# Optimization experiments

Hardware: AMD Instinct MI355X
Metric: run time of the kernel (lower is better)

## Reference

```python
import jax, jax.numpy as jnp
import numpy as np

N = 50000
E = 800000
BN_EPS = 1e-5


def setup_inputs() -> dict:
    key = jax.random.key(0)
    ks = jax.random.split(key, 8)
    x = jax.random.normal(ks[0], (N, 64), dtype=jnp.float32)
    edge_index = jax.random.randint(ks[1], (2, E), 0, N, dtype=jnp.int64)
    edge_attr = jax.random.uniform(ks[2], (E,), dtype=jnp.float32)
    # GraphConv layer 1: lin_rel (with bias) + lin_root (no bias), 64 -> 128
    W1_rel = jax.random.normal(ks[3], (64, 128), dtype=jnp.float32) / np.sqrt(64)
    b1 = jnp.zeros((128,), dtype=jnp.float32)
    W1_root = jax.random.normal(ks[4], (64, 128), dtype=jnp.float32) / np.sqrt(64)
    # BatchNorm1d(128) affine params
    gamma = jnp.ones((128,), dtype=jnp.float32)
    beta = jnp.zeros((128,), dtype=jnp.float32)
    # GraphConv layer 2: 128 -> 32
    W2_rel = jax.random.normal(ks[5], (128, 32), dtype=jnp.float32) / np.sqrt(128)
    b2 = jnp.zeros((32,), dtype=jnp.float32)
    W2_root = jax.random.normal(ks[6], (128, 32), dtype=jnp.float32) / np.sqrt(128)
    return {"x": x, "edge_attr": edge_attr, "W1_rel": W1_rel, "b1": b1,
            "W1_root": W1_root, "gamma": gamma, "beta": beta,
            "W2_rel": W2_rel, "b2": b2, "W2_root": W2_root,
            "edge_index": edge_index}


def graph_conv(x, edge_index, edge_weight, W_rel, b_rel, W_root):
    # PyG GraphConv (aggr='add'): out = lin_rel(scatter_add(w_e * x[src] -> dst)) + lin_root(x)
    src, dst = edge_index[0], edge_index[1]
    msg = x[src] * edge_weight[:, None]              # [E, F] gather + scale
    agg = jax.ops.segment_sum(msg, dst, num_segments=x.shape[0])  # [N, F]
    return agg @ W_rel + b_rel + x @ W_root


def batch_norm_train(h, gamma, beta):
    mean = jnp.mean(h, axis=0)
    var = jnp.var(h, axis=0)  # biased, as torch uses for normalization
    return (h - mean) * jax.lax.rsqrt(var + BN_EPS) * gamma + beta


def reference(x, edge_attr, W1_rel, b1, W1_root, gamma, beta, W2_rel, b2, W2_root, edge_index):
    h = graph_conv(x, edge_index, edge_attr, W1_rel, b1, W1_root)
    h = batch_norm_train(h, gamma, beta)
    h = jnp.tanh(h)
    out = graph_conv(h, edge_index, edge_attr, W2_rel, b2, W2_root)
    return out
```

## Files before the change

### kernel.cpp

```cpp
#include <hip/hip_runtime.h>
#include <hip/hip_bf16.h>


#define NB 256
#define CAPB 4096
#define LCAP 16
#define CHUNK 2048
#define CAP 32
#define MAXROWS 196
#define OVF_CAP 131072

typedef __bf16 bf16x8 __attribute__((ext_vector_type(8)));
typedef float f32x4 __attribute__((ext_vector_type(4)));

__device__ __forceinline__ void atomAdd(float* p, float v) { unsafeAtomicAdd(p, v); }

__device__ __forceinline__ unsigned packrec(unsigned src, float w) {
    __bf16 bw = (__bf16)w;
    unsigned short us = *(unsigned short*)&bw;
    return (src << 16) | (unsigned)us;
}

__global__ __launch_bounds__(256) void cvtw_k(
    const float* __restrict__ W1rel, const float* __restrict__ W1root,
    const float* __restrict__ W2rel, const float* __restrict__ W2root,
    const float* __restrict__ x,
    __bf16* __restrict__ W1t, __bf16* __restrict__ W2t, __bf16* __restrict__ xb,
    int* __restrict__ gcnt, int* __restrict__ ovfcnt,
    float* __restrict__ bnsum, float* __restrict__ bnsq, int N) {
    if (blockIdx.x == 0) {
        int t = threadIdx.x;
        if (t < NB) gcnt[t] = 0;
        if (t == 0) *ovfcnt = 0;
        if (t < 128) { bnsum[t] = 0.f; bnsq[t] = 0.f; }
    }
    int idx = blockIdx.x * 256 + threadIdx.x;
    if (idx < 128 * 128) {
        int n = idx >> 7, k = idx & 127;
        float v = (k < 64) ? W1rel[k * 128 + n] : W1root[(k - 64) * 128 + n];
        W1t[n * 128 + k] = (__bf16)v;
    } else if (idx < 128 * 128 + 64 * 128) {
        int j = idx - 128 * 128;
        int n = j >> 7, k = j & 127;
        float v = (n < 32) ? W2rel[k * 32 + n] : W2root[k * 32 + (n - 32)];
        W2t[n * 128 + k] = (__bf16)v;
    } else {
        int j = idx - (128 * 128 + 64 * 128);
        if (j < N * 8) {
            const float4* xs = (const float4*)(x + (size_t)j * 8);
            float4 a = xs[0], b = xs[1];
            bf16x8 v;
            v[0] = (__bf16)a.x; v[1] = (__bf16)a.y; v[2] = (__bf16)a.z; v[3] = (__bf16)a.w;
            v[4] = (__bf16)b.x; v[5] = (__bf16)b.y; v[6] = (__bf16)b.z; v[7] = (__bf16)b.w;
            *(bf16x8*)(xb + (size_t)j * 8) = v;
        }
    }
}

__global__ __launch_bounds__(256) void part_k(
    const float* __restrict__ ea, const void* __restrict__ ei,
    int* __restrict__ gcnt, uint2* __restrict__ part,
    int* __restrict__ ovfcnt, int4* __restrict__ ovf, int E, int N) {
    __shared__ int s_flag;
    __shared__ int hist[NB];
    __shared__ int gb[NB];
    __shared__ uint2 stage[NB * LCAP];

    if (threadIdx.x < 64) {
        const long long* p = (const long long*)ei;
        long long v = p[threadIdx.x & 15];
        int ok = (v >= 0 && v < (long long)N);
        unsigned long long m = __ballot(ok);
        if (threadIdx.x == 0) s_flag = (~m == 0ull) ? 1 : 0;
    }
    for (int i = threadIdx.x; i < NB; i += 256) hist[i] = 0;
    __syncthreads();
    const bool is64 = (s_flag != 0);

    const int base = blockIdx.x * CHUNK + threadIdx.x * 8;
    int n = E - base; n = n < 0 ? 0 : (n > 8 ? 8 : n);

    int srcs[8], dsts[8]; float wv[8];
    if (n > 0) {
        if (is64) {
            const long long* p = (const long long*)ei;
            if (n == 8 && ((E & 1) == 0)) {
#pragma unroll
                for (int k = 0; k < 4; k++) {
                    int4 a = *(const int4*)(p + base + 2 * k);
                    srcs[2 * k] = a.x; srcs[2 * k + 1] = a.z;
                }
#pragma unroll
                for (int k = 0; k < 4; k++) {
                    int4 b = *(const int4*)(p + E + base + 2 * k);
                    dsts[2 * k] = b.x; dsts[2 * k + 1] = b.z;
                }
            } else {
                for (int k = 0; k < n; k++) { srcs[k] = (int)p[base + k]; dsts[k] = (int)p[E + base + k]; }
            }
        } else {
            const int* p = (const int*)ei;
            if (n == 8 && ((E & 3) == 0)) {
                int4 a0 = *(const int4*)(p + base);
                int4 a1 = *(const int4*)(p + base + 4);
                srcs[0] = a0.x; srcs[1] = a0.y; srcs[2] = a0.z; srcs[3] = a0.w;
                srcs[4] = a1.x; srcs[5] = a1.y; srcs[6] = a1.z; srcs[7] = a1.w;
                int4 b0 = *(const int4*)(p + E + base);
                int4 b1 = *(const int4*)(p + E + base + 4);
                dsts[0] = b0.x; dsts[1] = b0.y; dsts[2] = b0.z; dsts[3] = b0.w;
                dsts[4] = b1.x; dsts[5] = b1.y; dsts[6] = b1.z; dsts[7] = b1.w;
            } else {
                for (int k = 0; k < n; k++) { srcs[k] = p[base + k]; dsts[k] = p[E + base + k]; }
            }
        }
        if (n == 8) {
            float4 w0 = *(const float4*)(ea + base);
            float4 w1 = *(const float4*)(ea + base + 4);
            wv[0] = w0.x; wv[1] = w0.y; wv[2] = w0.z; wv[3] = w0.w;
            wv[4] = w1.x; wv[5] = w1.y; wv[6] = w1.z; wv[7] = w1.w;
        } else {
            for (int k = 0; k < n; k++) wv[k] = ea[base + k];
        }

        int bk[8], pos[8], loc[8];
#pragma unroll
        for (int k = 0; k < 8; k++) {
            if (k < n) {
                unsigned b = ((unsigned)dsts[k] << 8) / (unsigned)N;
                int r0 = (int)((b * (unsigned)N + 255u) >> 8);
                bk[k] = (int)b;
                loc[k] = dsts[k] - r0;
                pos[k] = atomicAdd(&hist[b], 1);
            }
        }
#pragma unroll
        for (int k = 0; k < 8; k++) {
            if (k < n) {
                unsigned packed = ((unsigned)loc[k] << 24) | (unsigned)srcs[k];
                if (pos[k] < LCAP) {
                    stage[bk[k] * LCAP + pos[k]] = make_uint2(packed, __float_as_uint(wv[k]));
                } else {
                    int g = atomicAdd(&gcnt[bk[k]], 1);
                    if (g < CAPB) {
                        part[(size_t)bk[k] * CAPB + g] = make_uint2(packed, __float_as_uint(wv[k]));
                    } else {
                        int o = atomicAdd(ovfcnt, 1);
                        if (o < OVF_CAP) ovf[o] = make_int4(srcs[k], dsts[k], (int)__float_as_uint(wv[k]), 0);
                    }
                }
            }
        }
    }
    __syncthreads();
    if (threadIdx.x < NB) {
        int h = hist[threadIdx.x]; if (h > LCAP) h = LCAP;
        hist[threadIdx.x] = h;
        gb[threadIdx.x] = h ? atomicAdd(&gcnt[threadIdx.x], h) : 0;
    }
    __syncthreads();
    const int wvi = threadIdx.x >> 6;
    const int sub = (threadIdx.x >> 4) & 3;
    const int f = threadIdx.x & 15;
    for (int round = 0; round < 16; ++round) {
        int b = wvi * 64 + round * 4 + sub;
        int h = hist[b];
        if (f < h) {
            int g = gb[b] + f;
            uint2 r = stage[b * LCAP + f];
            if (g < CAPB) {
                part[(size_t)b * CAPB + g] = r;
            } else {
                int r0 = (b * N + 255) >> 8;
                int dst = r0 + (int)(r.x >> 24);
                int o = atomicAdd(ovfcnt, 1);
                if (o < OVF_CAP) ovf[o] = make_int4((int)(r.x & 0xFFFFFFu), dst, (int)r.y, 0);
            }
        }
    }
}

__global__ __launch_bounds__(256) void binscat_k(
    const int* __restrict__ gcnt, const uint2* __restrict__ part,
    unsigned* __restrict__ bins, int* __restrict__ cnt,
    int* __restrict__ ovfcnt, int4* __restrict__ ovf, int N) {
    __shared__ unsigned stage[MAXROWS * CAP];
    __shared__ int lcnt[MAXROWS];
    const int b = blockIdx.x;
    const int r0 = (b * N + 255) >> 8;
    int r1 = ((b + 1) * N + 255) >> 8; if (r1 > N) r1 = N;
    const int rows = r1 - r0;
    for (int i = threadIdx.x; i < rows; i += 256) lcnt[i] = 0;
    __syncthreads();

    int m = gcnt[b]; if (m > CAPB) m = CAPB;
    const uint2* pb = part + (size_t)b * CAPB;
    for (int i = threadIdx.x; i < m; i += 256) {
        uint2 r = pb[i];
        int d = r.x >> 24;
        unsigned src = r.x & 0xFFFFFFu;
        float w = __uint_as_float(r.y);
        int pos = atomicAdd(&lcnt[d], 1);
        if (pos < CAP) {
            stage[d * CAP + pos] = packrec(src, w);
        } else {
            int o = atomicAdd(ovfcnt, 1);
            if (o < OVF_CAP) ovf[o] = make_int4((int)src, r0 + d, (int)r.y, 0);
        }
    }
    __syncthreads();
    uint4* dst = (uint4*)(bins + (size_t)r0 * CAP);
    const uint4* srcp = (const uint4*)stage;
    for (int i = threadIdx.x; i < rows * (CAP / 4); i += 256) dst[i] = srcp[i];
    for (int i = threadIdx.x; i < rows; i += 256) cnt[r0 + i] = lcnt[i];
}

__global__ __launch_bounds__(256) void spmm1_k(
    const __bf16* __restrict__ xb, const int* __restrict__ cntg,
    const unsigned* __restrict__ bins, const int* __restrict__ ovfcnt,
    const int4* __restrict__ ovf, __bf16* __restrict__ aggb, int N) {
    const int lane = threadIdx.x & 63;
    const int row = (blockIdx.x * 256 + threadIdx.x) >> 6;
    if (row >= N) return;
    int cf = cntg[row];
    int cnt = cf > CAP ? CAP : cf;
    unsigned eg = 0u;
    if (lane < cnt) eg = bins[(size_t)row * CAP + lane];
    float acc = 0.f;
    for (int j = 0; j < cnt; j += 8) {
        int s[8]; float w[8], v[8];
#pragma unroll
        for (int k = 0; k < 8; k++) {
            int idx = j + k;
            bool ok = idx < cnt;
            unsigned r = (unsigned)__shfl((int)eg, idx);
            s[k] = ok ? (int)(r >> 16) : 0;
            w[k] = ok ? __uint_as_float((r & 0xFFFFu) << 16) : 0.f;
        }
#pragma unroll
        for (int k = 0; k < 8; k++) v[k] = (float)xb[(size_t)s[k] * 64 + lane];
#pragma unroll
        for (int k = 0; k < 8; k++) acc = fmaf(w[k], v[k], acc);
    }
    if (cf > CAP) {
        int nv = *ovfcnt; if (nv > OVF_CAP) nv = OVF_CAP;
        for (int i = 0; i < nv; i++) {
            int4 t = ovf[i];
            if (t.y == row) {
                float w = __uint_as_float((unsigned)t.z);
                acc = fmaf(w, (float)xb[(size_t)t.x * 64 + lane], acc);
            }
        }
    }
    aggb[(size_t)row * 64 + lane] = (__bf16)acc;
}

__global__ __launch_bounds__(256) void gemm1_k(
    const __bf16* __restrict__ aggb, const __bf16* __restrict__ xb,
    const __bf16* __restrict__ W1t, const float* __restrict__ b1,
    __bf16* __restrict__ hb, float* __restrict__ bnsum, float* __restrict__ bnsq,
    int N) {
    __shared__ char Wl[128 * 256];
    __shared__ float redS[4][128];
    __shared__ float redQ[4][128];
    const int t = threadIdx.x;
    for (int i = t; i < 2048; i += 256) {
        int byte = i * 16;
        int row = byte >> 8;
        int sw = byte ^ ((row & 7) << 4);
        *(uint4*)(Wl + sw) = *(const uint4*)((const char*)W1t + byte);
    }

    const int lane = t & 63;
    const int w = t >> 6;
    const int rrow = lane & 15;
    const int q = lane >> 4;
    const int rowbase = blockIdx.x * 128 + w * 32;
    const int ar0 = rowbase + rrow;
    const int ar1 = rowbase + 16 + rrow;
    const int ar0c = (ar0 < N) ? ar0 : (N - 1);
    const int ar1c = (ar1 < N) ? ar1 : (N - 1);

    f32x4 acc0[8], acc1[8];
#pragma unroll
    for (int cb = 0; cb < 8; cb++) {
        acc0[cb][0] = 0.f; acc0[cb][1] = 0.f; acc0[cb][2] = 0.f; acc0[cb][3] = 0.f;
        acc1[cb][0] = 0.f; acc1[cb][1] = 0.f; acc1[cb][2] = 0.f; acc1[cb][3] = 0.f;
    }
    __syncthreads();

#pragma unroll
    for (int ks = 0; ks < 4; ks++) {
        const int koff = (ks & 1) * 32 + q * 8;
        const __bf16* base = (ks < 2) ? aggb : xb;
        bf16x8 a0 = *(const bf16x8*)(base + (size_t)ar0c * 64 + koff);
        bf16x8 a1 = *(const bf16x8*)(base + (size_t)ar1c * 64 + koff);
#pragma unroll
        for (int cb = 0; cb < 8; cb++) {
            int byte = (cb * 16 + rrow) * 256 + ks * 64 + q * 16;
            byte ^= ((rrow & 7) << 4);
            bf16x8 b = *(const bf16x8*)(Wl + byte);
            acc0[cb] = __builtin_amdgcn_mfma_f32_16x16x32_bf16(a0, b, acc0[cb], 0, 0, 0);
            acc1[cb] = __builtin_amdgcn_mfma_f32_16x16x32_bf16(a1, b, acc1[cb], 0, 0, 0);
        }
    }

    float s[8], qs[8];
#pragma unroll
    for (int cb = 0; cb < 8; cb++) {
        const int col = cb * 16 + rrow;
        const float bc = b1[col];
        float ls = 0.f, lq = 0.f;
#pragma unroll
        for (int r = 0; r < 4; r++) {
            int rr0 = rowbase + 4 * q + r;
            if (rr0 < N) {
                float v = acc0[cb][r] + bc;
                hb[(size_t)rr0 * 128 + col] = (__bf16)v;
                ls += v; lq += v * v;
            }
            int rr1 = rowbase + 16 + 4 * q + r;
            if (rr1 < N) {
                float v = acc1[cb][r] + bc;
                hb[(size_t)rr1 * 128 + col] = (__bf16)v;
                ls += v; lq += v * v;
            }
        }
        s[cb] = ls; qs[cb] = lq;
    }
#pragma unroll
    for (int cb = 0; cb < 8; cb++) {
        s[cb] += __shfl_xor(s[cb], 16);  s[cb] += __shfl_xor(s[cb], 32);
        qs[cb] += __shfl_xor(qs[cb], 16); qs[cb] += __shfl_xor(qs[cb], 32);
    }
    if (q == 0) {
#pragma unroll
        for (int cb = 0; cb < 8; cb++) {
            redS[w][cb * 16 + rrow] = s[cb];
            redQ[w][cb * 16 + rrow] = qs[cb];
        }
    }
    __syncthreads();
    if (t < 128) {
        atomAdd(&bnsum[t], redS[0][t] + redS[1][t] + redS[2][t] + redS[3][t]);
    } else {
        int c = t - 128;
        atomAdd(&bnsq[c], redQ[0][c] + redQ[1][c] + redQ[2][c] + redQ[3][c]);
    }
}

__global__ __launch_bounds__(256) void gemm2_k(
    const __bf16* __restrict__ hb, const float* __restrict__ bnsum,
    const float* __restrict__ bnsq, const float* __restrict__ gamma,
    const float* __restrict__ beta, const __bf16* __restrict__ W2t,
    const float* __restrict__ b2, __bf16* __restrict__ y2b,
    float* __restrict__ out, int N) {
    __shared__ char Wl[64 * 256];
    __shared__ float scs[128], shs[128];
    const int t = threadIdx.x;
    for (int i = t; i < 1024; i += 256) {
        int byte = i * 16;
        int row = byte >> 8;
        int sw = byte ^ ((row & 7) << 4);
        *(uint4*)(Wl + sw) = *(const uint4*)((const char*)W2t + byte);
    }
    if (t < 128) {
        float inv = 1.0f / (float)N;
        float mean = bnsum[t] * inv;
        float var = bnsq[t] * inv - mean * mean;
        if (var < 0.f) var = 0.f;
        float sc = gamma[t] * rsqrtf(var + 1e-5f);
        scs[t] = sc;
        shs[t] = beta[t] - mean * sc;
    }

    const int lane = t & 63;
    const int w = t >> 6;
    const int rrow = lane & 15;
    const int q = lane >> 4;
    const int rowbase = blockIdx.x * 128 + w * 32;
    const int ar0 = rowbase + rrow;
    const int ar1 = rowbase + 16 + rrow;
    const int ar0c = (ar0 < N) ? ar0 : (N - 1);
    const int ar1c = (ar1 < N) ? ar1 : (N - 1);

    f32x4 acc0[4], acc1[4];
#pragma unroll
    for (int cb = 0; cb < 4; cb++) {
        acc0[cb][0] = 0.f; acc0[cb][1] = 0.f; acc0[cb][2] = 0.f; acc0[cb][3] = 0.f;
        acc1[cb][0] = 0.f; acc1[cb][1] = 0.f; acc1[cb][2] = 0.f; acc1[cb][3] = 0.f;
    }
    __syncthreads();

#pragma unroll
    for (int ks = 0; ks < 4; ks++) {
        const int k0 = ks * 32 + q * 8;
        bf16x8 hv0 = *(const bf16x8*)(hb + (size_t)ar0c * 128 + k0);
        bf16x8 hv1 = *(const bf16x8*)(hb + (size_t)ar1c * 128 + k0);
        bf16x8 a0, a1;
#pragma unroll
        for (int i = 0; i < 8; i++) {
            float sc = scs[k0 + i], sh = shs[k0 + i];
            a0[i] = (__bf16)tanhf(fmaf((float)hv0[i], sc, sh));
            a1[i] = (__bf16)tanhf(fmaf((float)hv1[i], sc, sh));
        }
#pragma unroll
        for (int cb = 0; cb < 4; cb++) {
            int byte = (cb * 16 + rrow) * 256 + ks * 64 + q * 16;
            byte ^= ((rrow & 7) << 4);
            bf16x8 b = *(const bf16x8*)(Wl + byte);
            acc0[cb] = __builtin_amdgcn_mfma_f32_16x16x32_bf16(a0, b, acc0[cb], 0, 0, 0);
            acc1[cb] = __builtin_amdgcn_mfma_f32_16x16x32_bf16(a1, b, acc1[cb], 0, 0, 0);
        }
    }

#pragma unroll
    for (int cb = 0; cb < 4; cb++) {
        const int col = cb * 16 + rrow;
        const bool isRel = (col < 32);
        const int cc = isRel ? col : (col - 32);
        const float bc = isRel ? 0.f : b2[cc];
#pragma unroll
        for (int r = 0; r < 4; r++) {
            int rr0 = rowbase + 4 * q + r;
            if (rr0 < N) {
                if (isRel) y2b[(size_t)rr0 * 32 + cc] = (__bf16)acc0[cb][r];
                else       out[(size_t)rr0 * 32 + cc] = acc0[cb][r] + bc;
            }
            int rr1 = rowbase + 16 + 4 * q + r;
            if (rr1 < N) {
                if (isRel) y2b[(size_t)rr1 * 32 + cc] = (__bf16)acc1[cb][r];
                else       out[(size_t)rr1 * 32 + cc] = acc1[cb][r] + bc;
            }
        }
    }
}

__global__ __launch_bounds__(256) void spmm2_k(
    const __bf16* __restrict__ y2b, const int* __restrict__ cntg,
    const unsigned* __restrict__ bins, const int* __restrict__ ovfcnt,
    const int4* __restrict__ ovf, float* __restrict__ out, int N) {
    const int lane = threadIdx.x & 63;
    const int f = lane & 31;
    const int sub = lane >> 5;
    const int row = (blockIdx.x * 256 + threadIdx.x) >> 6;
    if (row >= N) return;
    int cf = cntg[row];
    int cnt = cf > CAP ? CAP : cf;
    unsigned eg = 0u;
    if (lane < cnt) eg = bins[(size_t)row * CAP + lane];
    float acc = 0.f;
    for (int j = 0; j < cnt; j += 4) {
        int s[2]; float w[2], v[2];
#pragma unroll
        for (int k = 0; k < 2; k++) {
            int idx = j + 2 * k + sub;
            bool ok = idx < cnt;
            unsigned r = (unsigned)__shfl((int)eg, idx);
            s[k] = ok ? (int)(r >> 16) : 0;
            w[k] = ok ? __uint_as_float((r & 0xFFFFu) << 16) : 0.f;
        }
#pragma unroll
        for (int k = 0; k < 2; k++) v[k] = (float)y2b[(size_t)s[k] * 32 + f];
#pragma unroll
        for (int k = 0; k < 2; k++) acc = fmaf(w[k], v[k], acc);
    }
    if (cf > CAP && sub == 0) {
        int nv = *ovfcnt; if (nv > OVF_CAP) nv = OVF_CAP;
        for (int i = 0; i < nv; i++) {
            int4 t = ovf[i];
            if (t.y == row) {
                float w = __uint_as_float((unsigned)t.z);
                acc = fmaf(w, (float)y2b[(size_t)t.x * 32 + f], acc);
            }
        }
    }
    acc += __shfl_xor(acc, 32);
    if (sub == 0) {
        float* p = &out[(size_t)row * 32 + f];
        *p = *p + acc;
    }
}

extern "C" void kernel_launch(void* const* d_in, const int* in_sizes, int n_in,
                              void* d_out, int out_size, void* d_ws, size_t ws_size,
                              hipStream_t stream) {
    const float* x      = (const float*)d_in[0];
    const float* ea     = (const float*)d_in[1];
    const float* W1rel  = (const float*)d_in[2];
    const float* b1     = (const float*)d_in[3];
    const float* W1root = (const float*)d_in[4];
    const float* gamma  = (const float*)d_in[5];
    const float* beta   = (const float*)d_in[6];
    const float* W2rel  = (const float*)d_in[7];
    const float* b2     = (const float*)d_in[8];
    const float* W2root = (const float*)d_in[9];
    const void*  ei     = d_in[10];

    const int N = in_sizes[0] / 64;
    const int E = in_sizes[1];
    const int nbg = (N + 127) / 128;

    char* ws = (char*)d_ws;
    size_t off = 0;
    int*      gcnt    = (int*)     (ws + off); off += NB * 4;
    int*      ovfcnt  = (int*)     (ws + off); off += 256;
    float*    bnsum   = (float*)   (ws + off); off += 512;
    float*    bnsq    = (float*)   (ws + off); off += 512;
    int*      cnt     = (int*)     (ws + off); off += ((size_t)N * 4 + 255) & ~255ull;
    __bf16*   xb      = (__bf16*)  (ws + off); off += (size_t)N * 64 * 2;
    __bf16*   aggb    = (__bf16*)  (ws + off); off += (size_t)N * 64 * 2;
    __bf16*   hb      = (__bf16*)  (ws + off); off += (size_t)N * 128 * 2;
    __bf16*   y2b     = (__bf16*)  (ws + off); off += (size_t)N * 32 * 2;
    uint2*    part    = (uint2*)   (ws + off); off += (size_t)NB * CAPB * 8;
    unsigned* bins    = (unsigned*)(ws + off); off += (size_t)N * CAP * 4;
    int4*     ovf     = (int4*)    (ws + off); off += (size_t)OVF_CAP * 16;
    __bf16*   W1t     = (__bf16*)  (ws + off); off += 128 * 128 * 2;
    __bf16*   W2t     = (__bf16*)  (ws + off); off += 64 * 128 * 2;

    const int cvtThreads = 128 * 128 + 64 * 128 + N * 8;
    cvtw_k<<<(cvtThreads + 255) / 256, 256, 0, stream>>>(
        W1rel, W1root, W2rel, W2root, x, W1t, W2t, xb, gcnt, ovfcnt, bnsum, bnsq, N);
    part_k<<<(E + CHUNK - 1) / CHUNK, 256, 0, stream>>>(ea, ei, gcnt, part, ovfcnt, ovf, E, N);
    binscat_k<<<NB, 256, 0, stream>>>(gcnt, part, bins, cnt, ovfcnt, ovf, N);
    const int rowBlocks = (N * 64 + 255) / 256;
    spmm1_k<<<rowBlocks, 256, 0, stream>>>(xb, cnt, bins, ovfcnt, ovf, aggb, N);
    gemm1_k<<<nbg, 256, 0, stream>>>(aggb, xb, W1t, b1, hb, bnsum, bnsq, N);
    gemm2_k<<<nbg, 256, 0, stream>>>(hb, bnsum, bnsq, gamma, beta, W2t, b2, y2b,
                                     (float*)d_out, N);
    spmm2_k<<<rowBlocks, 256, 0, stream>>>(y2b, cnt, bins, ovfcnt, ovf, (float*)d_out, N);
}
```

Measured before the change: 117.6 us.

## Vectorize SpMM gathers to packed bf16 pairs and merge x conversion into partition kernel

Both SpMM kernels now load two bf16 features per lane as one 32-bit word and split the wavefront into sub-groups that handle different edges in parallel, then combine the partial sums with cross-lane shuffles. This cuts the number of gather instructions and widens each memory access. The x-to-bf16 conversion moves out of the weight-init kernel into extra leading blocks of the partition kernel, so that conversion can overlap with edge partitioning. The cost is extra shuffle reductions, and the conversion blocks enlarge a launch that also uses a lot of shared memory.

```diff
diff --git a/kernel.cpp b/kernel.cpp
--- a/kernel.cpp
+++ b/kernel.cpp
@@ -21,13 +21,12 @@
     return (src << 16) | (unsigned)us;
 }
 
-__global__ __launch_bounds__(256) void cvtw_k(
+__global__ __launch_bounds__(256) void init_k(
     const float* __restrict__ W1rel, const float* __restrict__ W1root,
     const float* __restrict__ W2rel, const float* __restrict__ W2root,
-    const float* __restrict__ x,
-    __bf16* __restrict__ W1t, __bf16* __restrict__ W2t, __bf16* __restrict__ xb,
+    __bf16* __restrict__ W1t, __bf16* __restrict__ W2t,
     int* __restrict__ gcnt, int* __restrict__ ovfcnt,
-    float* __restrict__ bnsum, float* __restrict__ bnsq, int N) {
+    float* __restrict__ bnsum, float* __restrict__ bnsq) {
     if (blockIdx.x == 0) {
         int t = threadIdx.x;
         if (t < NB) gcnt[t] = 0;
@@ -44,8 +43,21 @@
         int n = j >> 7, k = j & 127;
         float v = (n < 32) ? W2rel[k * 32 + n] : W2root[k * 32 + (n - 32)];
         W2t[n * 128 + k] = (__bf16)v;
-    } else {
-        int j = idx - (128 * 128 + 64 * 128);
+    }
+}
+
+__global__ __launch_bounds__(256) void partx_k(
+    const float* __restrict__ x, __bf16* __restrict__ xb, int xcB,
+    const float* __restrict__ ea, const void* __restrict__ ei,
+    int* __restrict__ gcnt, uint2* __restrict__ part,
+    int* __restrict__ ovfcnt, int4* __restrict__ ovf, int E, int N) {
+    __shared__ int s_flag;
+    __shared__ int hist[NB];
+    __shared__ int gb[NB];
+    __shared__ uint2 stage[NB * LCAP];
+
+    if ((int)blockIdx.x < xcB) {
+        int j = blockIdx.x * 256 + threadIdx.x;
         if (j < N * 8) {
             const float4* xs = (const float4*)(x + (size_t)j * 8);
             float4 a = xs[0], b = xs[1];
@@ -54,17 +66,9 @@
             v[4] = (__bf16)b.x; v[5] = (__bf16)b.y; v[6] = (__bf16)b.z; v[7] = (__bf16)b.w;
             *(bf16x8*)(xb + (size_t)j * 8) = v;
         }
-    }
-}
-
-__global__ __launch_bounds__(256) void part_k(
-    const float* __restrict__ ea, const void* __restrict__ ei,
-    int* __restrict__ gcnt, uint2* __restrict__ part,
-    int* __restrict__ ovfcnt, int4* __restrict__ ovf, int E, int N) {
-    __shared__ int s_flag;
-    __shared__ int hist[NB];
-    __shared__ int gb[NB];
-    __shared__ uint2 stage[NB * LCAP];
+        return;
+    }
+    const int pb = blockIdx.x - xcB;
 
     if (threadIdx.x < 64) {
         const long long* p = (const long long*)ei;
@@ -77,7 +81,7 @@
     __syncthreads();
     const bool is64 = (s_flag != 0);
 
-    const int base = blockIdx.x * CHUNK + threadIdx.x * 8;
+    const int base = pb * CHUNK + threadIdx.x * 8;
     int n = E - base; n = n < 0 ? 0 : (n > 8 ? 8 : n);
 
     int srcs[8], dsts[8]; float wv[8];
@@ -219,39 +223,54 @@
     const unsigned* __restrict__ bins, const int* __restrict__ ovfcnt,
     const int4* __restrict__ ovf, __bf16* __restrict__ aggb, int N) {
     const int lane = threadIdx.x & 63;
+    const int sub = lane >> 5;
+    const int fp = lane & 31;
     const int row = (blockIdx.x * 256 + threadIdx.x) >> 6;
     if (row >= N) return;
     int cf = cntg[row];
     int cnt = cf > CAP ? CAP : cf;
     unsigned eg = 0u;
     if (lane < cnt) eg = bins[(size_t)row * CAP + lane];
-    float acc = 0.f;
+    float ax = 0.f, ay = 0.f;
     for (int j = 0; j < cnt; j += 8) {
-        int s[8]; float w[8], v[8];
-#pragma unroll
-        for (int k = 0; k < 8; k++) {
-            int idx = j + k;
+        int ss[4]; float ww[4]; unsigned uv[4];
+#pragma unroll
+        for (int k = 0; k < 4; k++) {
+            int idx = j + 2 * k + sub;
             bool ok = idx < cnt;
             unsigned r = (unsigned)__shfl((int)eg, idx);
-            s[k] = ok ? (int)(r >> 16) : 0;
-            w[k] = ok ? __uint_as_float((r & 0xFFFFu) << 16) : 0.f;
-        }
-#pragma unroll
-        for (int k = 0; k < 8; k++) v[k] = (float)xb[(size_t)s[k] * 64 + lane];
-#pragma unroll
-        for (int k = 0; k < 8; k++) acc = fmaf(w[k], v[k], acc);
-    }
-    if (cf > CAP) {
+            ss[k] = ok ? (int)(r >> 16) : 0;
+            ww[k] = ok ? __uint_as_float((r & 0xFFFFu) << 16) : 0.f;
+        }
+#pragma unroll
+        for (int k = 0; k < 4; k++)
+            uv[k] = *(const unsigned*)((const char*)xb + (size_t)ss[k] * 128 + fp * 4);
+#pragma unroll
+        for (int k = 0; k < 4; k++) {
+            ax = fmaf(ww[k], __uint_as_float((uv[k] & 0xFFFFu) << 16), ax);
+            ay = fmaf(ww[k], __uint_as_float(uv[k] & 0xFFFF0000u), ay);
+        }
+    }
+    if (cf > CAP && sub == 0) {
         int nv = *ovfcnt; if (nv > OVF_CAP) nv = OVF_CAP;
         for (int i = 0; i < nv; i++) {
             int4 t = ovf[i];
             if (t.y == row) {
                 float w = __uint_as_float((unsigned)t.z);
-                acc = fmaf(w, (float)xb[(size_t)t.x * 64 + lane], acc);
-            }
-        }
-    }
-    aggb[(size_t)row * 64 + lane] = (__bf16)acc;
+                unsigned u = *(const unsigned*)((const char*)xb + (size_t)t.x * 128 + fp * 4);
+                ax = fmaf(w, __uint_as_float((u & 0xFFFFu) << 16), ax);
+                ay = fmaf(w, __uint_as_float(u & 0xFFFF0000u), ay);
+            }
+        }
+    }
+    ax += __shfl_xor(ax, 32);
+    ay += __shfl_xor(ay, 32);
+    if (sub == 0) {
+        __bf16 b0 = (__bf16)ax, b1 = (__bf16)ay;
+        unsigned pack = (unsigned)*(unsigned short*)&b0 |
+                        ((unsigned)*(unsigned short*)&b1 << 16);
+        *(unsigned*)((char*)aggb + (size_t)row * 128 + fp * 4) = pack;
+    }
 }
 
 __global__ __launch_bounds__(256) void gemm1_k(
@@ -440,44 +459,53 @@
     const unsigned* __restrict__ bins, const int* __restrict__ ovfcnt,
     const int4* __restrict__ ovf, float* __restrict__ out, int N) {
     const int lane = threadIdx.x & 63;
-    const int f = lane & 31;
-    const int sub = lane >> 5;
+    const int qs = lane >> 4;
+    const int fp = lane & 15;
     const int row = (blockIdx.x * 256 + threadIdx.x) >> 6;
     if (row >= N) return;
     int cf = cntg[row];
     int cnt = cf > CAP ? CAP : cf;
     unsigned eg = 0u;
     if (lane < cnt) eg = bins[(size_t)row * CAP + lane];
-    float acc = 0.f;
-    for (int j = 0; j < cnt; j += 4) {
-        int s[2]; float w[2], v[2];
+    float ax = 0.f, ay = 0.f;
+    for (int j = 0; j < cnt; j += 8) {
+        int ss[2]; float ww[2]; unsigned uv[2];
 #pragma unroll
         for (int k = 0; k < 2; k++) {
-            int idx = j + 2 * k + sub;
+            int idx = j + 4 * k + qs;
             bool ok = idx < cnt;
             unsigned r = (unsigned)__shfl((int)eg, idx);
-            s[k] = ok ? (int)(r >> 16) : 0;
-            w[k] = ok ? __uint_as_float((r & 0xFFFFu) << 16) : 0.f;
-        }
-#pragma unroll
-        for (int k = 0; k < 2; k++) v[k] = (float)y2b[(size_t)s[k] * 32 + f];
-#pragma unroll
-        for (int k = 0; k < 2; k++) acc = fmaf(w[k], v[k], acc);
-    }
-    if (cf > CAP && sub == 0) {
+            ss[k] = ok ? (int)(r >> 16) : 0;
+            ww[k] = ok ? __uint_as_float((r & 0xFFFFu) << 16) : 0.f;
+        }
+#pragma unroll
+        for (int k = 0; k < 2; k++)
+            uv[k] = *(const unsigned*)((const char*)y2b + (size_t)ss[k] * 64 + fp * 4);
+#pragma unroll
+        for (int k = 0; k < 2; k++) {
+            ax = fmaf(ww[k], __uint_as_float((uv[k] & 0xFFFFu) << 16), ax);
+            ay = fmaf(ww[k], __uint_as_float(uv[k] & 0xFFFF0000u), ay);
+        }
+    }
+    if (cf > CAP && qs == 0) {
         int nv = *ovfcnt; if (nv > OVF_CAP) nv = OVF_CAP;
         for (int i = 0; i < nv; i++) {
             int4 t = ovf[i];
             if (t.y == row) {
                 float w = __uint_as_float((unsigned)t.z);
-                acc = fmaf(w, (float)y2b[(size_t)t.x * 32 + f], acc);
-            }
-        }
-    }
-    acc += __shfl_xor(acc, 32);
-    if (sub == 0) {
-        float* p = &out[(size_t)row * 32 + f];
-        *p = *p + acc;
+                unsigned u = *(const unsigned*)((const char*)y2b + (size_t)t.x * 64 + fp * 4);
+                ax = fmaf(w, __uint_as_float((u & 0xFFFFu) << 16), ax);
+                ay = fmaf(w, __uint_as_float(u & 0xFFFF0000u), ay);
+            }
+        }
+    }
+    ax += __shfl_xor(ax, 16); ax += __shfl_xor(ax, 32);
+    ay += __shfl_xor(ay, 16); ay += __shfl_xor(ay, 32);
+    if (qs == 0) {
+        float2* p = (float2*)((char*)out + (size_t)row * 128 + fp * 8);
+        float2 c = *p;
+        c.x += ax; c.y += ay;
+        *p = c;
     }
 }
 
@@ -517,10 +545,12 @@
     __bf16*   W1t     = (__bf16*)  (ws + off); off += 128 * 128 * 2;
     __bf16*   W2t     = (__bf16*)  (ws + off); off += 64 * 128 * 2;
 
-    const int cvtThreads = 128 * 128 + 64 * 128 + N * 8;
-    cvtw_k<<<(cvtThreads + 255) / 256, 256, 0, stream>>>(
-        W1rel, W1root, W2rel, W2root, x, W1t, W2t, xb, gcnt, ovfcnt, bnsum, bnsq, N);
-    part_k<<<(E + CHUNK - 1) / CHUNK, 256, 0, stream>>>(ea, ei, gcnt, part, ovfcnt, ovf, E, N);
+    init_k<<<96, 256, 0, stream>>>(W1rel, W1root, W2rel, W2root, W1t, W2t,
+                                   gcnt, ovfcnt, bnsum, bnsq);
+    const int xcB = (N * 8 + 255) / 256;
+    const int partB = (E + CHUNK - 1) / CHUNK;
+    partx_k<<<xcB + partB, 256, 0, stream>>>(x, xb, xcB, ea, ei, gcnt, part,
+                                             ovfcnt, ovf, E, N);
     binscat_k<<<NB, 256, 0, stream>>>(gcnt, part, bins, cnt, ovfcnt, ovf, N);
     const int rowBlocks = (N * 64 + 255) / 256;
     spmm1_k<<<rowBlocks, 256, 0, stream>>>(xb, cnt, bins, ovfcnt, ovf, aggb, N);
```

After: 112.7 us (median of 2 runs). -4.2%, faster.
